# Kernel tuning notes

Hardware: AMD Instinct MI355X
Metric: run time of the kernel (lower is better)

## Reference

```python
import jax, jax.numpy as jnp
import numpy as np

N = 16384
E = 524288
C = 16

def setup_inputs() -> dict:
    key = jax.random.key(0)
    ks = jax.random.split(key, 8)
    x = jax.random.normal(ks[0], (N, N), dtype=jnp.float32)
    edge_index = jax.random.randint(ks[1], (2, E), 0, N, dtype=jnp.int64)
    def glorot(k, fi, fo):
        s = jnp.sqrt(6.0 / (fi + fo)).astype(jnp.float32)
        return jax.random.uniform(k, (fi, fo), jnp.float32, -s, s)
    return {
        "x": x,
        "edge_index": edge_index,
        "W1": glorot(ks[2], N, 64),  "b1": jnp.zeros((64,), jnp.float32),
        "W2": glorot(ks[3], 64, 32), "b2": jnp.zeros((32,), jnp.float32),
        "W3": glorot(ks[4], 32, C),  "b3": jnp.zeros((C,), jnp.float32),
    }

def _gcn_norm(edge_index, n):
    # add self loops, compute symmetric normalization (PyG gcn_norm)
    loops = jnp.arange(n, dtype=edge_index.dtype)
    row = jnp.concatenate([edge_index[0], loops])  # source
    col = jnp.concatenate([edge_index[1], loops])  # target (aggregation index)
    deg = jax.ops.segment_sum(jnp.ones_like(col, dtype=jnp.float32), col, num_segments=n)
    dis = jnp.where(deg > 0, jax.lax.rsqrt(deg), 0.0)
    norm = dis[row] * dis[col]  # [E+N]
    return row, col, norm

def _gcn_conv(h, row, col, norm, W, b, n):
    h = h @ W                              # [N, F_out]
    msg = h[row] * norm[:, None]           # gather + scale per edge
    out = jax.ops.segment_sum(msg, col, num_segments=n)  # scatter-add at targets
    return out + b

def reference(x, edge_index, W1, b1, W2, b2, W3, b3):
    n = x.shape[0]
    row, col, norm = _gcn_norm(edge_index, n)
    h = jax.nn.relu(_gcn_conv(x, row, col, norm, W1, b1, n))
    h = jax.nn.relu(_gcn_conv(h, row, col, norm, W2, b2, n))
    h = _gcn_conv(h, row, col, norm, W3, b3, n)
    return jax.nn.softmax(h, axis=1)
```

## Files before the change

kernel.cpp:

```cpp
#include <hip/hip_runtime.h>


typedef __attribute__((ext_vector_type(8))) short bf16x8;
typedef __attribute__((ext_vector_type(4))) float f32x4;
typedef __attribute__((ext_vector_type(4))) float fv4;

__device__ __forceinline__ float4 ldnt4(const float* p) {
    fv4 v = __builtin_nontemporal_load((const fv4*)p);
    return make_float4(v.x, v.y, v.z, v.w);
}
__device__ __forceinline__ void stnt(float* p, float v) {
    __builtin_nontemporal_store(v, p);
}

__device__ __forceinline__ unsigned cvt_pk_bf16(float a, float b) {
    unsigned r;
    asm("v_cvt_pk_bf16_f32 %0, %1, %2" : "=v"(r) : "v"(a), "v"(b));
    return r;
}

__device__ __forceinline__ unsigned short f2bf_rne(float f) {
    unsigned u = __float_as_uint(f);
    unsigned r = (u + 0x7FFFu + ((u >> 16) & 1u)) >> 16;
    return (unsigned short)r;
}

__global__ void init_prep_k(const int* __restrict__ ei, int* __restrict__ flag,
                            int* __restrict__ cnt, int n,
                            const float* __restrict__ W1,
                            unsigned short* __restrict__ Bt, int K) {
    int t = blockIdx.x * blockDim.x + threadIdx.x;
    if (t < n) cnt[t] = 0;
    if (t == 0) {
        int f = 1;
        for (int i = 0; i < 256; ++i) {
            if (ei[2 * i + 1] != 0) { f = 0; break; }
        }
        *flag = f;
    }
    if (t < K * 64) {
        int nn = t & 63, k = t >> 6;
        float f = W1[(size_t)k * 64 + nn];
        unsigned short hi = f2bf_rne(f);
        float hf = __uint_as_float((unsigned)hi << 16);
        unsigned short lo = f2bf_rne(f - hf);
        Bt[(size_t)nn * K + k] = hi;
        Bt[(size_t)64 * K + (size_t)nn * K + k] = lo;
    }
}

__device__ __forceinline__ int edge_val(const int* __restrict__ ei, long long idx, int f64) {
    return f64 ? ei[2 * idx] : ei[(int)idx];
}

__global__ void count_deg_k(const int* __restrict__ ei, int E, const int* __restrict__ flag,
                            int* __restrict__ cnt) {
    int e = blockIdx.x * blockDim.x + threadIdx.x;
    if (e >= E) return;
    int f = *flag;
    int c = edge_val(ei, (long long)E + e, f);
    atomicAdd(&cnt[c], 1);
}

__global__ void scan_blk_k(const int* __restrict__ cnt, int* __restrict__ offs,
                           float* __restrict__ dis, int* __restrict__ cursor,
                           int* __restrict__ btot, int n) {
    __shared__ int sh[256];
    const int t = threadIdx.x;
    const int idx = blockIdx.x * 256 + t;
    int v = (idx < n) ? cnt[idx] : 0;
    sh[t] = v;
    __syncthreads();
    for (int o = 1; o < 256; o <<= 1) {
        int add = (t >= o) ? sh[t - o] : 0;
        __syncthreads();
        sh[t] += add;
        __syncthreads();
    }
    if (idx < n) {
        offs[idx] = sh[t] - v;
        cursor[idx] = 0;
        dis[idx] = rsqrtf((float)(v + 1));
    }
    if (t == 255) btot[blockIdx.x] = sh[255];
}

__global__ void scan_top_k(int* __restrict__ btot, int* __restrict__ offs, int nb, int n) {
    __shared__ int sh[64];
    const int t = threadIdx.x;
    int v = (t < nb) ? btot[t] : 0;
    sh[t] = v;
    __syncthreads();
    for (int o = 1; o < 64; o <<= 1) {
        int add = (t >= o) ? sh[t - o] : 0;
        __syncthreads();
        sh[t] += add;
        __syncthreads();
    }
    if (t < nb) btot[t] = sh[t] - v;
    if (t == nb - 1) offs[n] = sh[t];
}

__global__ void scan_add_k(int* __restrict__ offs, const int* __restrict__ btot, int n) {
    int idx = blockIdx.x * 256 + threadIdx.x;
    if (idx < n) offs[idx] += btot[blockIdx.x];
}

__global__ void fill_csr_k(const int* __restrict__ ei, int E, const int* __restrict__ flag,
                           const int* __restrict__ offs, int* __restrict__ cursor,
                           const float* __restrict__ dis, int* __restrict__ src,
                           float* __restrict__ w) {
    int e = blockIdx.x * blockDim.x + threadIdx.x;
    if (e >= E) return;
    int f = *flag;
    int r = edge_val(ei, (long long)e, f);
    int c = edge_val(ei, (long long)E + e, f);
    int pos = offs[c] + atomicAdd(&cursor[c], 1);
    src[pos] = r;
    w[pos] = dis[r] * dis[c];
}

__global__ __launch_bounds__(256) void gemm1_mfma_k(
    const float* __restrict__ A, const unsigned short* __restrict__ Bt,
    float* __restrict__ P, int n, int K, int kchunk) {
    __shared__ unsigned short As[2][128][40];
    const int tid = threadIdx.x;
    const int lane = tid & 63;
    const int wid = tid >> 6;
    const int wm = wid >> 1, wn = wid & 1;
    const int lrow = lane & 15, lkh = lane >> 4;
    const int bid = blockIdx.x;
    const int by = (bid & 7) >> 1;
    const int bx = ((bid >> 3) << 1) | (bid & 1);
    const int bm = bx * 128;
    const int k0 = by * kchunk;
    const int iters = kchunk / 32;

    const unsigned short* Bh = Bt;
    const unsigned short* Bl = Bt + (size_t)64 * K;

    f32x4 acc[4][2] = {};
    float4 st[4];

    auto loadA = [&](int kt) {
#pragma unroll
        for (int i = 0; i < 4; ++i) {
            int v = tid + i * 256;
            int r = v >> 3, c = (v & 7) * 4;
            st[i] = ldnt4(A + (size_t)(bm + r) * K + k0 + kt * 32 + c);
        }
    };

    loadA(0);
    for (int kt = 0; kt < iters; ++kt) {
        bf16x8 bh[2], bl[2];
#pragma unroll
        for (int nf = 0; nf < 2; ++nf) {
            int brow = wn * 32 + nf * 16 + lrow;
            size_t bo = (size_t)brow * K + k0 + kt * 32 + lkh * 8;
            bh[nf] = *(const bf16x8*)(Bh + bo);
            bl[nf] = *(const bf16x8*)(Bl + bo);
        }
#pragma unroll
        for (int i = 0; i < 4; ++i) {
            int v = tid + i * 256;
            int r = v >> 3, c = (v & 7) * 4;
            float f0 = st[i].x, f1 = st[i].y, f2 = st[i].z, f3 = st[i].w;
            unsigned h01 = cvt_pk_bf16(f0, f1);
            unsigned h23 = cvt_pk_bf16(f2, f3);
            float r0 = f0 - __uint_as_float(h01 << 16);
            float r1 = f1 - __uint_as_float(h01 & 0xFFFF0000u);
            float r2 = f2 - __uint_as_float(h23 << 16);
            float r3 = f3 - __uint_as_float(h23 & 0xFFFF0000u);
            unsigned l01 = cvt_pk_bf16(r0, r1);
            unsigned l23 = cvt_pk_bf16(r2, r3);
            *(uint2*)&As[0][r][c] = make_uint2(h01, h23);
            *(uint2*)&As[1][r][c] = make_uint2(l01, l23);
        }
        __syncthreads();
        if (kt + 1 < iters) loadA(kt + 1);
        bf16x8 ah[4], al[4];
#pragma unroll
        for (int mf = 0; mf < 4; ++mf) {
            int row = wm * 64 + mf * 16 + lrow;
            ah[mf] = *(const bf16x8*)&As[0][row][lkh * 8];
            al[mf] = *(const bf16x8*)&As[1][row][lkh * 8];
        }
#pragma unroll
        for (int mf = 0; mf < 4; ++mf)
#pragma unroll
            for (int nf = 0; nf < 2; ++nf) {
                acc[mf][nf] = __builtin_amdgcn_mfma_f32_16x16x32_bf16(ah[mf], bh[nf], acc[mf][nf], 0, 0, 0);
                acc[mf][nf] = __builtin_amdgcn_mfma_f32_16x16x32_bf16(al[mf], bh[nf], acc[mf][nf], 0, 0, 0);
                acc[mf][nf] = __builtin_amdgcn_mfma_f32_16x16x32_bf16(ah[mf], bl[nf], acc[mf][nf], 0, 0, 0);
            }
        __syncthreads();
    }
    float* out = P + (size_t)by * n * 64;
#pragma unroll
    for (int mf = 0; mf < 4; ++mf)
#pragma unroll
        for (int nf = 0; nf < 2; ++nf)
#pragma unroll
            for (int j = 0; j < 4; ++j) {
                int row = bm + wm * 64 + mf * 16 + lkh * 4 + j;
                int col = wn * 32 + nf * 16 + lrow;
                stnt(out + (size_t)row * 64 + col, acc[mf][nf][j]);
            }
}

__global__ void reduce4_k(float4* __restrict__ p, size_t q) {
    size_t i = (size_t)blockIdx.x * blockDim.x + threadIdx.x;
    if (i >= q) return;
    float4 a = p[i];
#pragma unroll
    for (int z = 1; z < 4; ++z) {
        float4 b = ldnt4((const float*)(p + i + (size_t)z * q));
        a.x += b.x; a.y += b.y; a.z += b.z; a.w += b.w;
    }
    p[i] = a;
}

__global__ __launch_bounds__(256) void prop64_gemm2_k(
    const float* __restrict__ h, const int* __restrict__ offs,
    const int* __restrict__ src, const float* __restrict__ w,
    const float* __restrict__ dis, const float* __restrict__ b1,
    const float* __restrict__ W2, float* __restrict__ H2a, int n) {
    __shared__ float Ws[64 * 32];
    __shared__ float rows[16][68];
    const int tid = threadIdx.x;
    for (int i = tid; i < 64 * 32; i += 256) Ws[i] = W2[i];
    const int t = blockIdx.x * 256 + tid;
    const int node = t >> 4, q = t & 15, nl = tid >> 4;
    float4 acc = make_float4(0.f, 0.f, 0.f, 0.f);
    int p0 = offs[node], p1 = offs[node + 1];
    for (int p = p0; p < p1; ++p) {
        float ww = w[p];
        float4 hv = *(const float4*)(h + (size_t)src[p] * 64 + q * 4);
        acc.x = fmaf(ww, hv.x, acc.x);
        acc.y = fmaf(ww, hv.y, acc.y);
        acc.z = fmaf(ww, hv.z, acc.z);
        acc.w = fmaf(ww, hv.w, acc.w);
    }
    float d = dis[node];
    float ds = d * d;
    float4 hv = *(const float4*)(h + (size_t)node * 64 + q * 4);
    float4 bv = *(const float4*)(b1 + q * 4);
    acc.x = fmaxf(fmaf(ds, hv.x, acc.x) + bv.x, 0.f);
    acc.y = fmaxf(fmaf(ds, hv.y, acc.y) + bv.y, 0.f);
    acc.z = fmaxf(fmaf(ds, hv.z, acc.z) + bv.z, 0.f);
    acc.w = fmaxf(fmaf(ds, hv.w, acc.w) + bv.w, 0.f);
    *(float4*)&rows[nl][q * 4] = acc;
    __syncthreads();
    const int c0 = q * 2;
    float s0 = 0.f, s1 = 0.f;
#pragma unroll
    for (int k = 0; k < 64; ++k) {
        float v = rows[nl][k];
        s0 = fmaf(v, Ws[k * 32 + c0], s0);
        s1 = fmaf(v, Ws[k * 32 + c0 + 1], s1);
    }
    H2a[(size_t)node * 32 + c0] = s0;
    H2a[(size_t)node * 32 + c0 + 1] = s1;
}

__global__ __launch_bounds__(256) void prop32_gemm3_k(
    const float* __restrict__ h, const int* __restrict__ offs,
    const int* __restrict__ src, const float* __restrict__ w,
    const float* __restrict__ dis, const float* __restrict__ b2,
    const float* __restrict__ W3, float* __restrict__ H3a, int n) {
    __shared__ float Ws[32 * 16];
    __shared__ float rows[32][36];
    const int tid = threadIdx.x;
    for (int i = tid; i < 32 * 16; i += 256) Ws[i] = W3[i];
    const int t = blockIdx.x * 256 + tid;
    const int node = t >> 3, q = t & 7, nl = tid >> 3;
    float4 acc = make_float4(0.f, 0.f, 0.f, 0.f);
    int p0 = offs[node], p1 = offs[node + 1];
    for (int p = p0; p < p1; ++p) {
        float ww = w[p];
        float4 hv = *(const float4*)(h + (size_t)src[p] * 32 + q * 4);
        acc.x = fmaf(ww, hv.x, acc.x);
        acc.y = fmaf(ww, hv.y, acc.y);
        acc.z = fmaf(ww, hv.z, acc.z);
        acc.w = fmaf(ww, hv.w, acc.w);
    }
    float d = dis[node];
    float ds = d * d;
    float4 hv = *(const float4*)(h + (size_t)node * 32 + q * 4);
    float4 bv = *(const float4*)(b2 + q * 4);
    acc.x = fmaxf(fmaf(ds, hv.x, acc.x) + bv.x, 0.f);
    acc.y = fmaxf(fmaf(ds, hv.y, acc.y) + bv.y, 0.f);
    acc.z = fmaxf(fmaf(ds, hv.z, acc.z) + bv.z, 0.f);
    acc.w = fmaxf(fmaf(ds, hv.w, acc.w) + bv.w, 0.f);
    *(float4*)&rows[nl][q * 4] = acc;
    __syncthreads();
    const int c0 = q * 2;
    float s0 = 0.f, s1 = 0.f;
#pragma unroll
    for (int k = 0; k < 32; ++k) {
        float v = rows[nl][k];
        s0 = fmaf(v, Ws[k * 16 + c0], s0);
        s1 = fmaf(v, Ws[k * 16 + c0 + 1], s1);
    }
    H3a[(size_t)node * 16 + c0] = s0;
    H3a[(size_t)node * 16 + c0 + 1] = s1;
}

__global__ void prop_softmax_k(const float* __restrict__ h, const int* __restrict__ offs,
                               const int* __restrict__ src, const float* __restrict__ w,
                               const float* __restrict__ dis, const float* __restrict__ b,
                               float* __restrict__ out, int n) {
    int t = blockIdx.x * blockDim.x + threadIdx.x;
    int node = t >> 2, q = t & 3;
    if (node >= n) return;
    float4 acc = make_float4(0.f, 0.f, 0.f, 0.f);
    int p0 = offs[node], p1 = offs[node + 1];
    for (int p = p0; p < p1; ++p) {
        float ww = w[p];
        float4 hv = *(const float4*)(h + (size_t)src[p] * 16 + q * 4);
        acc.x = fmaf(ww, hv.x, acc.x);
        acc.y = fmaf(ww, hv.y, acc.y);
        acc.z = fmaf(ww, hv.z, acc.z);
        acc.w = fmaf(ww, hv.w, acc.w);
    }
    float d = dis[node];
    float ds = d * d;
    float4 hv = *(const float4*)(h + (size_t)node * 16 + q * 4);
    float4 bv = *(const float4*)(b + q * 4);
    acc.x = fmaf(ds, hv.x, acc.x) + bv.x;
    acc.y = fmaf(ds, hv.y, acc.y) + bv.y;
    acc.z = fmaf(ds, hv.z, acc.z) + bv.z;
    acc.w = fmaf(ds, hv.w, acc.w) + bv.w;
    float m = fmaxf(fmaxf(acc.x, acc.y), fmaxf(acc.z, acc.w));
    m = fmaxf(m, __shfl_xor(m, 1));
    m = fmaxf(m, __shfl_xor(m, 2));
    float4 e;
    e.x = __expf(acc.x - m);
    e.y = __expf(acc.y - m);
    e.z = __expf(acc.z - m);
    e.w = __expf(acc.w - m);
    float s = e.x + e.y + e.z + e.w;
    s += __shfl_xor(s, 1);
    s += __shfl_xor(s, 2);
    float inv = 1.f / s;
    e.x *= inv; e.y *= inv; e.z *= inv; e.w *= inv;
    *(float4*)(out + (size_t)node * 16 + q * 4) = e;
}

extern "C" void kernel_launch(void* const* d_in, const int* in_sizes, int n_in,
                              void* d_out, int out_size, void* d_ws, size_t ws_size,
                              hipStream_t stream) {
    const float* x  = (const float*)d_in[0];
    const int*   ei = (const int*)d_in[1];
    const float* W1 = (const float*)d_in[2];
    const float* b1 = (const float*)d_in[3];
    const float* W2 = (const float*)d_in[4];
    const float* b2 = (const float*)d_in[5];
    const float* W3 = (const float*)d_in[6];
    const float* b3 = (const float*)d_in[7];
    float* out = (float*)d_out;

    const int n = in_sizes[2] / 64;
    const int K = in_sizes[0] / n;
    const int E = in_sizes[1] / 2;
    const int nb = (n + 255) / 256;

    char* ws = (char*)d_ws;
    size_t off = 0;
    auto alloc = [&](size_t bytes) {
        char* p = ws + off;
        off = (off + bytes + 255) & ~(size_t)255;
        return p;
    };
    int*   flag   = (int*)  alloc(4);
    int*   cnt    = (int*)  alloc((size_t)n * 4);
    int*   cursor = (int*)  alloc((size_t)n * 4);
    int*   offs   = (int*)  alloc((size_t)(n + 1) * 4);
    int*   btot   = (int*)  alloc((size_t)nb * 4);
    float* dis    = (float*)alloc((size_t)n * 4);
    int*   csrs   = (int*)  alloc((size_t)E * 4);
    float* csrw   = (float*)alloc((size_t)E * 4);
    unsigned short* Btw = (unsigned short*)alloc((size_t)2 * 64 * K * 2);
    float* P      = (float*)alloc((size_t)4 * n * 64 * 4);
    float* H2a    = (float*)alloc((size_t)n * 32 * 4);
    float* H3a    = (float*)alloc((size_t)n * 16 * 4);
    (void)ws_size; (void)n_in; (void)out_size;

    init_prep_k<<<(K * 64 + 255) / 256, 256, 0, stream>>>(ei, flag, cnt, n, W1, Btw, K);
    count_deg_k<<<(E + 255) / 256, 256, 0, stream>>>(ei, E, flag, cnt);
    scan_blk_k<<<nb, 256, 0, stream>>>(cnt, offs, dis, cursor, btot, n);
    scan_top_k<<<1, 64, 0, stream>>>(btot, offs, nb, n);
    scan_add_k<<<nb, 256, 0, stream>>>(offs, btot, n);
    fill_csr_k<<<(E + 255) / 256, 256, 0, stream>>>(ei, E, flag, offs, cursor, dis, csrs, csrw);

    gemm1_mfma_k<<<(n / 128) * 4, 256, 0, stream>>>(x, Btw, P, n, K, K / 4);
    size_t q = (size_t)n * 64 / 4;
    reduce4_k<<<(int)((q + 255) / 256), 256, 0, stream>>>((float4*)P, q);

    prop64_gemm2_k<<<n * 16 / 256, 256, 0, stream>>>(P, offs, csrs, csrw, dis, b1, W2, H2a, n);
    prop32_gemm3_k<<<n * 8 / 256, 256, 0, stream>>>(H2a, offs, csrs, csrw, dis, b2, W3, H3a, n);
    prop_softmax_k<<<n * 4 / 256, 256, 0, stream>>>(H3a, offs, csrs, csrw, dis, b3, out, n);
}
```

Before: 368.1 us.

## Use single-wave 32-row GEMM tiles without barriers and fuse scan top-level pass

The first-layer GEMM goes from 256-thread blocks covering 128 rows to 64-thread single-wavefront blocks covering 32 rows and all 64 output columns. With one wave per block, the two __syncthreads barriers per K-step can be removed, and four times as many blocks are launched to raise occupancy and hide the streaming of x. Each wave now loads twice as many B fragments per row tile, which adds B traffic and register pressure. Separately, the scan_top_k kernel is folded into scan_add_k: thread 0 of each block serially sums the block totals, saving one launch at the cost of redundant serial reads.

```diff
diff --git a/kernel.cpp b/kernel.cpp
--- a/kernel.cpp
+++ b/kernel.cpp
@@ -85,25 +85,24 @@
     if (t == 255) btot[blockIdx.x] = sh[255];
 }
 
-__global__ void scan_top_k(int* __restrict__ btot, int* __restrict__ offs, int nb, int n) {
-    __shared__ int sh[64];
+__global__ void scan_add_k(int* __restrict__ offs, const int* __restrict__ btot,
+                           int n, int nb) {
+    __shared__ int base_sh, tot_sh;
     const int t = threadIdx.x;
-    int v = (t < nb) ? btot[t] : 0;
-    sh[t] = v;
+    if (t == 0) {
+        int base = 0, tot = 0;
+        for (int i = 0; i < nb; ++i) {
+            int v = btot[i];
+            if (i < (int)blockIdx.x) base += v;
+            tot += v;
+        }
+        base_sh = base;
+        tot_sh = tot;
+    }
     __syncthreads();
-    for (int o = 1; o < 64; o <<= 1) {
-        int add = (t >= o) ? sh[t - o] : 0;
-        __syncthreads();
-        sh[t] += add;
-        __syncthreads();
-    }
-    if (t < nb) btot[t] = sh[t] - v;
-    if (t == nb - 1) offs[n] = sh[t];
-}
-
-__global__ void scan_add_k(int* __restrict__ offs, const int* __restrict__ btot, int n) {
-    int idx = blockIdx.x * 256 + threadIdx.x;
-    if (idx < n) offs[idx] += btot[blockIdx.x];
+    int idx = blockIdx.x * 256 + t;
+    if (idx < n) offs[idx] += base_sh;
+    if (blockIdx.x == 0 && t == 0) offs[n] = tot_sh;
 }
 
 __global__ void fill_csr_k(const int* __restrict__ ei, int E, const int* __restrict__ flag,
@@ -120,32 +119,29 @@
     w[pos] = dis[r] * dis[c];
 }
 
-__global__ __launch_bounds__(256) void gemm1_mfma_k(
+__global__ __launch_bounds__(64) void gemm1_mfma_k(
     const float* __restrict__ A, const unsigned short* __restrict__ Bt,
     float* __restrict__ P, int n, int K, int kchunk) {
-    __shared__ unsigned short As[2][128][40];
-    const int tid = threadIdx.x;
-    const int lane = tid & 63;
-    const int wid = tid >> 6;
-    const int wm = wid >> 1, wn = wid & 1;
+    __shared__ unsigned short As[2][32][40];
+    const int lane = threadIdx.x;
     const int lrow = lane & 15, lkh = lane >> 4;
     const int bid = blockIdx.x;
     const int by = (bid & 7) >> 1;
     const int bx = ((bid >> 3) << 1) | (bid & 1);
-    const int bm = bx * 128;
+    const int bm = bx * 32;
     const int k0 = by * kchunk;
     const int iters = kchunk / 32;
 
     const unsigned short* Bh = Bt;
     const unsigned short* Bl = Bt + (size_t)64 * K;
 
-    f32x4 acc[4][2] = {};
+    f32x4 acc[2][4] = {};
     float4 st[4];
 
     auto loadA = [&](int kt) {
 #pragma unroll
         for (int i = 0; i < 4; ++i) {
-            int v = tid + i * 256;
+            int v = lane + i * 64;
             int r = v >> 3, c = (v & 7) * 4;
             st[i] = ldnt4(A + (size_t)(bm + r) * K + k0 + kt * 32 + c);
         }
@@ -153,17 +149,17 @@
 
     loadA(0);
     for (int kt = 0; kt < iters; ++kt) {
-        bf16x8 bh[2], bl[2];
-#pragma unroll
-        for (int nf = 0; nf < 2; ++nf) {
-            int brow = wn * 32 + nf * 16 + lrow;
+        bf16x8 bh[4], bl[4];
+#pragma unroll
+        for (int nf = 0; nf < 4; ++nf) {
+            int brow = nf * 16 + lrow;
             size_t bo = (size_t)brow * K + k0 + kt * 32 + lkh * 8;
             bh[nf] = *(const bf16x8*)(Bh + bo);
             bl[nf] = *(const bf16x8*)(Bl + bo);
         }
 #pragma unroll
         for (int i = 0; i < 4; ++i) {
-            int v = tid + i * 256;
+            int v = lane + i * 64;
             int r = v >> 3, c = (v & 7) * 4;
             float f0 = st[i].x, f1 = st[i].y, f2 = st[i].z, f3 = st[i].w;
             unsigned h01 = cvt_pk_bf16(f0, f1);
@@ -177,34 +173,32 @@
             *(uint2*)&As[0][r][c] = make_uint2(h01, h23);
             *(uint2*)&As[1][r][c] = make_uint2(l01, l23);
         }
-        __syncthreads();
         if (kt + 1 < iters) loadA(kt + 1);
-        bf16x8 ah[4], al[4];
-#pragma unroll
-        for (int mf = 0; mf < 4; ++mf) {
-            int row = wm * 64 + mf * 16 + lrow;
+        bf16x8 ah[2], al[2];
+#pragma unroll
+        for (int mf = 0; mf < 2; ++mf) {
+            int row = mf * 16 + lrow;
             ah[mf] = *(const bf16x8*)&As[0][row][lkh * 8];
             al[mf] = *(const bf16x8*)&As[1][row][lkh * 8];
         }
 #pragma unroll
-        for (int mf = 0; mf < 4; ++mf)
-#pragma unroll
-            for (int nf = 0; nf < 2; ++nf) {
+        for (int mf = 0; mf < 2; ++mf)
+#pragma unroll
+            for (int nf = 0; nf < 4; ++nf) {
                 acc[mf][nf] = __builtin_amdgcn_mfma_f32_16x16x32_bf16(ah[mf], bh[nf], acc[mf][nf], 0, 0, 0);
                 acc[mf][nf] = __builtin_amdgcn_mfma_f32_16x16x32_bf16(al[mf], bh[nf], acc[mf][nf], 0, 0, 0);
                 acc[mf][nf] = __builtin_amdgcn_mfma_f32_16x16x32_bf16(ah[mf], bl[nf], acc[mf][nf], 0, 0, 0);
             }
-        __syncthreads();
     }
     float* out = P + (size_t)by * n * 64;
 #pragma unroll
-    for (int mf = 0; mf < 4; ++mf)
-#pragma unroll
-        for (int nf = 0; nf < 2; ++nf)
+    for (int mf = 0; mf < 2; ++mf)
+#pragma unroll
+        for (int nf = 0; nf < 4; ++nf)
 #pragma unroll
             for (int j = 0; j < 4; ++j) {
-                int row = bm + wm * 64 + mf * 16 + lkh * 4 + j;
-                int col = wn * 32 + nf * 16 + lrow;
+                int row = bm + mf * 16 + lkh * 4 + j;
+                int col = nf * 16 + lrow;
                 stnt(out + (size_t)row * 64 + col, acc[mf][nf][j]);
             }
 }
@@ -390,11 +384,10 @@
     init_prep_k<<<(K * 64 + 255) / 256, 256, 0, stream>>>(ei, flag, cnt, n, W1, Btw, K);
     count_deg_k<<<(E + 255) / 256, 256, 0, stream>>>(ei, E, flag, cnt);
     scan_blk_k<<<nb, 256, 0, stream>>>(cnt, offs, dis, cursor, btot, n);
-    scan_top_k<<<1, 64, 0, stream>>>(btot, offs, nb, n);
-    scan_add_k<<<nb, 256, 0, stream>>>(offs, btot, n);
+    scan_add_k<<<nb, 256, 0, stream>>>(offs, btot, n, nb);
     fill_csr_k<<<(E + 255) / 256, 256, 0, stream>>>(ei, E, flag, offs, cursor, dis, csrs, csrw);
 
-    gemm1_mfma_k<<<(n / 128) * 4, 256, 0, stream>>>(x, Btw, P, n, K, K / 4);
+    gemm1_mfma_k<<<(n / 32) * 4, 64, 0, stream>>>(x, Btw, P, n, K, K / 4);
     size_t q = (size_t)n * 64 / 4;
     reduce4_k<<<(int)((q + 255) / 256), 256, 0, stream>>>((float4*)P, q);
 
```

Measured after the change: 531.2 us. 44.3% more time.

## Double GEMM1 K-tile to 64 and fold top-level scan into scan_add

Applied to the files above, without the earlier changes.

The x@W1 split-bf16 MFMA GEMM now stages a 64-wide K slab per iteration instead of 32. That halves the number of barrier-synchronised iterations and doubles the in-flight global loads per thread, at the cost of more registers and LDS. Separately, the single-block top-level scan kernel is removed. Each scan_add block now serially sums the block totals itself, dropping one kernel launch.

```diff
diff --git a/kernel.cpp b/kernel.cpp
--- a/kernel.cpp
+++ b/kernel.cpp
@@ -85,25 +85,24 @@
     if (t == 255) btot[blockIdx.x] = sh[255];
 }
 
-__global__ void scan_top_k(int* __restrict__ btot, int* __restrict__ offs, int nb, int n) {
-    __shared__ int sh[64];
+__global__ void scan_add_k(int* __restrict__ offs, const int* __restrict__ btot,
+                           int n, int nb) {
+    __shared__ int base_sh, tot_sh;
     const int t = threadIdx.x;
-    int v = (t < nb) ? btot[t] : 0;
-    sh[t] = v;
+    if (t == 0) {
+        int base = 0, tot = 0;
+        for (int i = 0; i < nb; ++i) {
+            int v = btot[i];
+            if (i < (int)blockIdx.x) base += v;
+            tot += v;
+        }
+        base_sh = base;
+        tot_sh = tot;
+    }
     __syncthreads();
-    for (int o = 1; o < 64; o <<= 1) {
-        int add = (t >= o) ? sh[t - o] : 0;
-        __syncthreads();
-        sh[t] += add;
-        __syncthreads();
-    }
-    if (t < nb) btot[t] = sh[t] - v;
-    if (t == nb - 1) offs[n] = sh[t];
-}
-
-__global__ void scan_add_k(int* __restrict__ offs, const int* __restrict__ btot, int n) {
-    int idx = blockIdx.x * 256 + threadIdx.x;
-    if (idx < n) offs[idx] += btot[blockIdx.x];
+    int idx = blockIdx.x * 256 + t;
+    if (idx < n) offs[idx] += base_sh;
+    if (blockIdx.x == 0 && t == 0) offs[n] = tot_sh;
 }
 
 __global__ void fill_csr_k(const int* __restrict__ ei, int E, const int* __restrict__ flag,
@@ -123,7 +122,7 @@
 __global__ __launch_bounds__(256) void gemm1_mfma_k(
     const float* __restrict__ A, const unsigned short* __restrict__ Bt,
     float* __restrict__ P, int n, int K, int kchunk) {
-    __shared__ unsigned short As[2][128][40];
+    __shared__ unsigned short As[2][128][72];
     const int tid = threadIdx.x;
     const int lane = tid & 63;
     const int wid = tid >> 6;
@@ -134,37 +133,39 @@
     const int bx = ((bid >> 3) << 1) | (bid & 1);
     const int bm = bx * 128;
     const int k0 = by * kchunk;
-    const int iters = kchunk / 32;
+    const int iters = kchunk / 64;
 
     const unsigned short* Bh = Bt;
     const unsigned short* Bl = Bt + (size_t)64 * K;
 
     f32x4 acc[4][2] = {};
-    float4 st[4];
+    float4 st[8];
 
     auto loadA = [&](int kt) {
 #pragma unroll
-        for (int i = 0; i < 4; ++i) {
+        for (int i = 0; i < 8; ++i) {
             int v = tid + i * 256;
-            int r = v >> 3, c = (v & 7) * 4;
-            st[i] = ldnt4(A + (size_t)(bm + r) * K + k0 + kt * 32 + c);
+            int r = v >> 4, c = (v & 15) * 4;
+            st[i] = ldnt4(A + (size_t)(bm + r) * K + k0 + kt * 64 + c);
         }
     };
 
     loadA(0);
     for (int kt = 0; kt < iters; ++kt) {
-        bf16x8 bh[2], bl[2];
-#pragma unroll
-        for (int nf = 0; nf < 2; ++nf) {
-            int brow = wn * 32 + nf * 16 + lrow;
-            size_t bo = (size_t)brow * K + k0 + kt * 32 + lkh * 8;
-            bh[nf] = *(const bf16x8*)(Bh + bo);
-            bl[nf] = *(const bf16x8*)(Bl + bo);
-        }
-#pragma unroll
-        for (int i = 0; i < 4; ++i) {
+        bf16x8 bh[2][2], bl[2][2];
+#pragma unroll
+        for (int ks = 0; ks < 2; ++ks)
+#pragma unroll
+            for (int nf = 0; nf < 2; ++nf) {
+                int brow = wn * 32 + nf * 16 + lrow;
+                size_t bo = (size_t)brow * K + k0 + kt * 64 + ks * 32 + lkh * 8;
+                bh[ks][nf] = *(const bf16x8*)(Bh + bo);
+                bl[ks][nf] = *(const bf16x8*)(Bl + bo);
+            }
+#pragma unroll
+        for (int i = 0; i < 8; ++i) {
             int v = tid + i * 256;
-            int r = v >> 3, c = (v & 7) * 4;
+            int r = v >> 4, c = (v & 15) * 4;
             float f0 = st[i].x, f1 = st[i].y, f2 = st[i].z, f3 = st[i].w;
             unsigned h01 = cvt_pk_bf16(f0, f1);
             unsigned h23 = cvt_pk_bf16(f2, f3);
@@ -179,21 +180,24 @@
         }
         __syncthreads();
         if (kt + 1 < iters) loadA(kt + 1);
-        bf16x8 ah[4], al[4];
-#pragma unroll
-        for (int mf = 0; mf < 4; ++mf) {
-            int row = wm * 64 + mf * 16 + lrow;
-            ah[mf] = *(const bf16x8*)&As[0][row][lkh * 8];
-            al[mf] = *(const bf16x8*)&As[1][row][lkh * 8];
+#pragma unroll
+        for (int ks = 0; ks < 2; ++ks) {
+            bf16x8 ah[4], al[4];
+#pragma unroll
+            for (int mf = 0; mf < 4; ++mf) {
+                int row = wm * 64 + mf * 16 + lrow;
+                ah[mf] = *(const bf16x8*)&As[0][row][ks * 32 + lkh * 8];
+                al[mf] = *(const bf16x8*)&As[1][row][ks * 32 + lkh * 8];
+            }
+#pragma unroll
+            for (int mf = 0; mf < 4; ++mf)
+#pragma unroll
+                for (int nf = 0; nf < 2; ++nf) {
+                    acc[mf][nf] = __builtin_amdgcn_mfma_f32_16x16x32_bf16(ah[mf], bh[ks][nf], acc[mf][nf], 0, 0, 0);
+                    acc[mf][nf] = __builtin_amdgcn_mfma_f32_16x16x32_bf16(al[mf], bh[ks][nf], acc[mf][nf], 0, 0, 0);
+                    acc[mf][nf] = __builtin_amdgcn_mfma_f32_16x16x32_bf16(ah[mf], bl[ks][nf], acc[mf][nf], 0, 0, 0);
+                }
         }
-#pragma unroll
-        for (int mf = 0; mf < 4; ++mf)
-#pragma unroll
-            for (int nf = 0; nf < 2; ++nf) {
-                acc[mf][nf] = __builtin_amdgcn_mfma_f32_16x16x32_bf16(ah[mf], bh[nf], acc[mf][nf], 0, 0, 0);
-                acc[mf][nf] = __builtin_amdgcn_mfma_f32_16x16x32_bf16(al[mf], bh[nf], acc[mf][nf], 0, 0, 0);
-                acc[mf][nf] = __builtin_amdgcn_mfma_f32_16x16x32_bf16(ah[mf], bl[nf], acc[mf][nf], 0, 0, 0);
-            }
         __syncthreads();
     }
     float* out = P + (size_t)by * n * 64;
@@ -390,8 +394,7 @@
     init_prep_k<<<(K * 64 + 255) / 256, 256, 0, stream>>>(ei, flag, cnt, n, W1, Btw, K);
     count_deg_k<<<(E + 255) / 256, 256, 0, stream>>>(ei, E, flag, cnt);
     scan_blk_k<<<nb, 256, 0, stream>>>(cnt, offs, dis, cursor, btot, n);
-    scan_top_k<<<1, 64, 0, stream>>>(btot, offs, nb, n);
-    scan_add_k<<<nb, 256, 0, stream>>>(offs, btot, n);
+    scan_add_k<<<nb, 256, 0, stream>>>(offs, btot, n, nb);
     fill_csr_k<<<(E + 255) / 256, 256, 0, stream>>>(ei, E, flag, offs, cursor, dis, csrs, csrw);
 
     gemm1_mfma_k<<<(n / 128) * 4, 256, 0, stream>>>(x, Btw, P, n, K, K / 4);
```

Measured after the change: 382.3 us. 1.04x slower.
